# Performance work log

Hardware: AMD Instinct MI355X
Metric: run time of the kernel (lower is better)

The kernel has to match this reference:

```python
import jax, jax.numpy as jnp
import numpy as np

T, B, D, H = 4096, 4, 1024, 16


def setup_inputs() -> dict:
    key = jax.random.key(0)
    k0, k1, k2 = jax.random.split(key, 3)
    x = jax.random.normal(k0, (T, B, D), jnp.float32)
    Wqkv = jax.random.normal(k1, (3 * D, D), jnp.float32) * 0.02
    bqkv = jnp.zeros((3 * D,), jnp.float32)
    Wout = jax.random.normal(k2, (D, D), jnp.float32) * 0.02
    bout = jnp.zeros((D,), jnp.float32)
    return {"x": x, "Wqkv": Wqkv, "bqkv": bqkv, "Wout": Wout, "bout": bout, "nhead": H}


def reference(x, Wqkv, bqkv, Wout, bout, nhead):
    # x: (T, B, D) seq-first, query is key is value
    T_, B_, D_ = x.shape
    hd = D_ // nhead
    qkv = x @ Wqkv.T + bqkv                      # (T, B, 3D)
    q, k, v = jnp.split(qkv, 3, axis=-1)         # each (T, B, D)

    def heads(t):                                 # -> (B, H, T, hd)
        return t.reshape(T_, B_, nhead, hd).transpose(1, 2, 0, 3)

    q, k, v = heads(q), heads(k), heads(v)

    # Pearson correlation over the sequence axis: X, Y are (B, H, hd, T)
    X = jnp.swapaxes(q, -2, -1)
    Y = jnp.swapaxes(k, -2, -1)
    Xc = X - X.mean(-1, keepdims=True)
    Yc = Y - Y.mean(-1, keepdims=True)
    c = jnp.einsum('bhdt,bhet->bhde', Xc, Yc)    # (B, H, hd, hd)
    sx = (Xc ** 2).sum(-1)                       # (B, H, hd)
    sy = (Yc ** 2).sum(-1)                       # (B, H, hd)
    std = jnp.sqrt(sx[..., :, None] * sy[..., None, :])
    corr = jnp.clip(c / std, -1.0, 1.0)          # (B, H, hd, hd)

    attn = jnp.einsum('bhtd,bhde->bhte', v, corr)  # v @ corr: (B, H, T, hd)
    out = attn.transpose(2, 0, 1, 3).reshape(T_, B_, D_)  # (T, B, D)
    return out @ Wout.T + bout
```

## Files before the change

kernel.cpp:

```cpp
#include <hip/hip_runtime.h>
#include <hip/hip_bf16.h>

#define TDIM 4096
#define BDIM 4
#define DDIM 1024
#define HDIM 16
#define HD   64
#define MDIM (TDIM * BDIM)

typedef __attribute__((ext_vector_type(8))) short short8v;
typedef __attribute__((ext_vector_type(4))) float f32x4;

__device__ __forceinline__ ushort f2bfu(float f) {
  union { __hip_bfloat16 h; ushort u; } c;
  c.h = __float2bfloat16(f);
  return c.u;
}
__device__ __forceinline__ float bfu2f(ushort u) {
  union { ushort u; __hip_bfloat16 h; } c;
  c.u = u;
  return __bfloat162float(c.h);
}

#define GLOAD16(gp, lp) __builtin_amdgcn_global_load_lds( \
    (const __attribute__((address_space(1))) void*)(gp),  \
    (__attribute__((address_space(3))) void*)(lp), 16, 0, 0)

__global__ __launch_bounds__(256)
void split_f32(const float* __restrict__ in, ushort* __restrict__ hi,
               ushort* __restrict__ lo, int n4)
{
  int i = blockIdx.x * blockDim.x + threadIdx.x;
  const int stride = gridDim.x * blockDim.x;
  for (; i < n4; i += stride) {
    const float4 v = ((const float4*)in)[i];
    ushort4 h, l;
    h.x = f2bfu(v.x); l.x = f2bfu(v.x - bfu2f(h.x));
    h.y = f2bfu(v.y); l.y = f2bfu(v.y - bfu2f(h.y));
    h.z = f2bfu(v.z); l.z = f2bfu(v.z - bfu2f(h.z));
    h.w = f2bfu(v.w); l.w = f2bfu(v.w - bfu2f(h.w));
    ((ushort4*)hi)[i] = h;
    ((ushort4*)lo)[i] = l;
  }
}

__global__ __launch_bounds__(256, 2)
void gemm1_mfma(const float* __restrict__ X, const ushort* __restrict__ Wh,
                const ushort* __restrict__ Wl, const float* __restrict__ bias,
                float* __restrict__ QK, ushort* __restrict__ Vh,
                ushort* __restrict__ Vl)
{
  __shared__ ushort sAh[128][32], sAl[128][32], sBh[128][32], sBl[128][32];
  const int tid = threadIdx.x;
  const int lane = tid & 63, wid = tid >> 6;
  const int m0 = blockIdx.y * 128, n0 = blockIdx.x * 128;
  const int ar = tid >> 3, aq = tid & 7;
  const int wm = wid >> 1, wn = wid & 1;
  const int fr = lane & 15, kg = lane >> 4;

  f32x4 acc[4][4];
#pragma unroll
  for (int m = 0; m < 4; ++m)
#pragma unroll
    for (int n = 0; n < 4; ++n) acc[m][n] = (f32x4){0.f, 0.f, 0.f, 0.f};

  for (int k0 = 0; k0 < DDIM; k0 += 32) {
    float4 av[4];
#pragma unroll
    for (int i = 0; i < 4; ++i)
      av[i] = *(const float4*)&X[(size_t)(m0 + ar + i * 32) * DDIM + k0 + aq * 4];
#pragma unroll
    for (int j = 0; j < 4; ++j) {
      const int c = wid * 4 + j;
      const int r0 = (c & 7) * 16;
      const int row = r0 + (lane >> 2);
      const int s = lane & 3;
      const size_t goff = (size_t)(n0 + row) * DDIM + k0 + ((s ^ (row & 3)) << 3);
      if (c < 8) GLOAD16(Wh + goff, &sBh[r0][0]);
      else       GLOAD16(Wl + goff, &sBl[r0][0]);
    }
#pragma unroll
    for (int i = 0; i < 4; ++i) {
      const int row = ar + i * 32;
      const int sl = (((aq >> 1) ^ (row & 3)) << 3) + ((aq & 1) << 2);
      ushort4 hv, lv;
      hv.x = f2bfu(av[i].x); lv.x = f2bfu(av[i].x - bfu2f(hv.x));
      hv.y = f2bfu(av[i].y); lv.y = f2bfu(av[i].y - bfu2f(hv.y));
      hv.z = f2bfu(av[i].z); lv.z = f2bfu(av[i].z - bfu2f(hv.z));
      hv.w = f2bfu(av[i].w); lv.w = f2bfu(av[i].w - bfu2f(hv.w));
      *(ushort4*)&sAh[row][sl] = hv;
      *(ushort4*)&sAl[row][sl] = lv;
    }
    __syncthreads();

    short8v ah[4], al[4], bh[4], bl[4];
#pragma unroll
    for (int m = 0; m < 4; ++m) {
      const int row = wm * 64 + m * 16 + fr;
      const int so = (kg ^ (row & 3)) << 3;
      ah[m] = *(const short8v*)&sAh[row][so];
      al[m] = *(const short8v*)&sAl[row][so];
    }
#pragma unroll
    for (int n = 0; n < 4; ++n) {
      const int col = wn * 64 + n * 16 + fr;
      const int so = (kg ^ (col & 3)) << 3;
      bh[n] = *(const short8v*)&sBh[col][so];
      bl[n] = *(const short8v*)&sBl[col][so];
    }
#pragma unroll
    for (int m = 0; m < 4; ++m)
#pragma unroll
      for (int n = 0; n < 4; ++n) {
        acc[m][n] = __builtin_amdgcn_mfma_f32_16x16x32_bf16(ah[m], bh[n], acc[m][n], 0, 0, 0);
        acc[m][n] = __builtin_amdgcn_mfma_f32_16x16x32_bf16(ah[m], bl[n], acc[m][n], 0, 0, 0);
        acc[m][n] = __builtin_amdgcn_mfma_f32_16x16x32_bf16(al[m], bh[n], acc[m][n], 0, 0, 0);
      }
    __syncthreads();
  }

  const int isV = (n0 >= 2048);
#pragma unroll
  for (int m = 0; m < 4; ++m)
#pragma unroll
    for (int n = 0; n < 4; ++n) {
      const int col = n0 + wn * 64 + n * 16 + fr;
      const float bz = bias[col];
#pragma unroll
      for (int r = 0; r < 4; ++r) {
        const int row = m0 + wm * 64 + m * 16 + kg * 4 + r;
        const float v = acc[m][n][r] + bz;
        if (!isV) {
          QK[(size_t)row * 2048 + col] = v;
        } else {
          const size_t o = (size_t)row * 1024 + (col - 2048);
          const ushort h = f2bfu(v);
          Vh[o] = h;
          Vl[o] = f2bfu(v - bfu2f(h));
        }
      }
    }
}

__global__ __launch_bounds__(256, 2)
void gemm2_mfma(const ushort* __restrict__ Vh, const ushort* __restrict__ Vl,
                const ushort* __restrict__ Weh, const ushort* __restrict__ Wel,
                const float* __restrict__ bias, float* __restrict__ Out)
{
  __shared__ ushort sAh[128][32], sAl[128][32], sBh[128][32], sBl[128][32];
  const int tid = threadIdx.x;
  const int lane = tid & 63, wid = tid >> 6;
  const int m0 = blockIdx.y * 128, n0 = blockIdx.x * 128, bb = blockIdx.z;
  const int wm = wid >> 1, wn = wid & 1;
  const int fr = lane & 15, kg = lane >> 4;

  f32x4 acc[4][4];
#pragma unroll
  for (int m = 0; m < 4; ++m)
#pragma unroll
    for (int n = 0; n < 4; ++n) acc[m][n] = (f32x4){0.f, 0.f, 0.f, 0.f};

  const size_t wB = (size_t)bb * DDIM * DDIM;

  for (int k0 = 0; k0 < DDIM; k0 += 32) {
#pragma unroll
    for (int j = 0; j < 8; ++j) {
      const int r0 = j * 16;
      const int row = r0 + (lane >> 2);
      const int s = lane & 3;
      const int ks = k0 + ((s ^ (row & 3)) << 3);
      if (wid == 0)
        GLOAD16(Vh + (size_t)((m0 + row) * 4 + bb) * 1024 + ks, &sAh[r0][0]);
      else if (wid == 1)
        GLOAD16(Vl + (size_t)((m0 + row) * 4 + bb) * 1024 + ks, &sAl[r0][0]);
      else if (wid == 2)
        GLOAD16(Weh + wB + (size_t)(n0 + row) * 1024 + ks, &sBh[r0][0]);
      else
        GLOAD16(Wel + wB + (size_t)(n0 + row) * 1024 + ks, &sBl[r0][0]);
    }
    __syncthreads();

    short8v ah[4], al[4], bh[4], bl[4];
#pragma unroll
    for (int m = 0; m < 4; ++m) {
      const int row = wm * 64 + m * 16 + fr;
      const int so = (kg ^ (row & 3)) << 3;
      ah[m] = *(const short8v*)&sAh[row][so];
      al[m] = *(const short8v*)&sAl[row][so];
    }
#pragma unroll
    for (int n = 0; n < 4; ++n) {
      const int col = wn * 64 + n * 16 + fr;
      const int so = (kg ^ (col & 3)) << 3;
      bh[n] = *(const short8v*)&sBh[col][so];
      bl[n] = *(const short8v*)&sBl[col][so];
    }
#pragma unroll
    for (int m = 0; m < 4; ++m)
#pragma unroll
      for (int n = 0; n < 4; ++n) {
        acc[m][n] = __builtin_amdgcn_mfma_f32_16x16x32_bf16(ah[m], bh[n], acc[m][n], 0, 0, 0);
        acc[m][n] = __builtin_amdgcn_mfma_f32_16x16x32_bf16(ah[m], bl[n], acc[m][n], 0, 0, 0);
        acc[m][n] = __builtin_amdgcn_mfma_f32_16x16x32_bf16(al[m], bh[n], acc[m][n], 0, 0, 0);
      }
    __syncthreads();
  }

  float* Ob = Out + (size_t)bb * 1024;
#pragma unroll
  for (int m = 0; m < 4; ++m)
#pragma unroll
    for (int n = 0; n < 4; ++n) {
      const int col = n0 + wn * 64 + n * 16 + fr;
      const float bz = bias[col];
#pragma unroll
      for (int r = 0; r < 4; ++r) {
        const int row = m0 + wm * 64 + m * 16 + kg * 4 + r;
        Ob[(size_t)row * 4096 + col] = acc[m][n][r] + bz;
      }
    }
}

__global__ __launch_bounds__(64)
void corr_partial(const float* __restrict__ QK, float* __restrict__ P)
{
  __shared__ float qs[32][64];
  __shared__ float ks[32][64];
  const int bh  = blockIdx.x;
  const int seg = blockIdx.y;
  const int b = bh >> 4;
  const int h = bh & 15;
  const int lane = threadIdx.x;
  const float* qb = QK + (size_t)b * 2048 + h * HD;
  const float* kb = qb + 1024;
  const int ty = lane >> 3;
  const int tx = lane & 7;
  const int rr = lane >> 4;
  const int cq = lane & 15;

  float acc[8][8];
#pragma unroll
  for (int i = 0; i < 8; ++i)
#pragma unroll
    for (int j = 0; j < 8; ++j) acc[i][j] = 0.f;
  float sQ[4]  = {0,0,0,0}, sK[4]  = {0,0,0,0};
  float sQ2[4] = {0,0,0,0}, sK2[4] = {0,0,0,0};

  for (int c = 0; c < 8; ++c) {
    const int tbase = seg * 256 + c * 32;
    float4 qv[8], kv[8];
#pragma unroll
    for (int i = 0; i < 8; ++i) {
      const size_t g = (size_t)(tbase + rr + i*4) * 8192 + cq * 4;
      qv[i] = *(const float4*)&qb[g];
      kv[i] = *(const float4*)&kb[g];
    }
    __syncthreads();
#pragma unroll
    for (int i = 0; i < 8; ++i) {
      const int row = rr + i*4;
      *(float4*)&qs[row][cq*4] = qv[i];
      *(float4*)&ks[row][cq*4] = kv[i];
      sQ[0] += qv[i].x; sQ[1] += qv[i].y; sQ[2] += qv[i].z; sQ[3] += qv[i].w;
      sK[0] += kv[i].x; sK[1] += kv[i].y; sK[2] += kv[i].z; sK[3] += kv[i].w;
      sQ2[0] = fmaf(qv[i].x, qv[i].x, sQ2[0]); sQ2[1] = fmaf(qv[i].y, qv[i].y, sQ2[1]);
      sQ2[2] = fmaf(qv[i].z, qv[i].z, sQ2[2]); sQ2[3] = fmaf(qv[i].w, qv[i].w, sQ2[3]);
      sK2[0] = fmaf(kv[i].x, kv[i].x, sK2[0]); sK2[1] = fmaf(kv[i].y, kv[i].y, sK2[1]);
      sK2[2] = fmaf(kv[i].z, kv[i].z, sK2[2]); sK2[3] = fmaf(kv[i].w, kv[i].w, sK2[3]);
    }
    __syncthreads();
#pragma unroll 8
    for (int t = 0; t < 32; ++t) {
      const float4 qa  = *(const float4*)&qs[t][ty*8];
      const float4 qb4 = *(const float4*)&qs[t][ty*8+4];
      const float4 ka  = *(const float4*)&ks[t][tx*8];
      const float4 kb4 = *(const float4*)&ks[t][tx*8+4];
      const float av[8] = {qa.x, qa.y, qa.z, qa.w, qb4.x, qb4.y, qb4.z, qb4.w};
      const float bv[8] = {ka.x, ka.y, ka.z, ka.w, kb4.x, kb4.y, kb4.z, kb4.w};
#pragma unroll
      for (int i = 0; i < 8; ++i)
#pragma unroll
        for (int j = 0; j < 8; ++j)
          acc[i][j] = fmaf(av[i], bv[j], acc[i][j]);
    }
  }

#pragma unroll
  for (int j = 0; j < 4; ++j) {
    sQ[j]  += __shfl_xor(sQ[j], 16, 64);  sQ[j]  += __shfl_xor(sQ[j], 32, 64);
    sK[j]  += __shfl_xor(sK[j], 16, 64);  sK[j]  += __shfl_xor(sK[j], 32, 64);
    sQ2[j] += __shfl_xor(sQ2[j], 16, 64); sQ2[j] += __shfl_xor(sQ2[j], 32, 64);
    sK2[j] += __shfl_xor(sK2[j], 16, 64); sK2[j] += __shfl_xor(sK2[j], 32, 64);
  }

  float* Pb = P + (size_t)(bh * 16 + seg) * 4352;
#pragma unroll
  for (int i = 0; i < 8; ++i) {
    const int row = ty*8 + i;
    float4 o0, o1;
    o0.x = acc[i][0]; o0.y = acc[i][1]; o0.z = acc[i][2]; o0.w = acc[i][3];
    o1.x = acc[i][4]; o1.y = acc[i][5]; o1.z = acc[i][6]; o1.w = acc[i][7];
    *(float4*)&Pb[row*64 + tx*8]     = o0;
    *(float4*)&Pb[row*64 + tx*8 + 4] = o1;
  }
  if (lane < 16) {
    float4 q4; q4.x = sQ[0];  q4.y = sQ[1];  q4.z = sQ[2];  q4.w = sQ[3];
    float4 k4; k4.x = sK[0];  k4.y = sK[1];  k4.z = sK[2];  k4.w = sK[3];
    float4 q2; q2.x = sQ2[0]; q2.y = sQ2[1]; q2.z = sQ2[2]; q2.w = sQ2[3];
    float4 k2; k2.x = sK2[0]; k2.y = sK2[1]; k2.z = sK2[2]; k2.w = sK2[3];
    *(float4*)&Pb[4096 + lane*4] = q4;
    *(float4*)&Pb[4160 + lane*4] = k4;
    *(float4*)&Pb[4224 + lane*4] = q2;
    *(float4*)&Pb[4288 + lane*4] = k2;
  }
}

__global__ __launch_bounds__(256)
void corr_finalize(const float* __restrict__ P, float* __restrict__ corr)
{
  __shared__ float fin[4][64];
  const int bh = blockIdx.x;
  const int tid = threadIdx.x;
  const float* Pb = P + (size_t)bh * 16 * 4352;

  float s = 0.f;
  for (int seg = 0; seg < 16; ++seg) s += Pb[(size_t)seg*4352 + 4096 + tid];
  fin[tid >> 6][tid & 63] = s;

  float cacc[16];
#pragma unroll
  for (int i = 0; i < 16; ++i) cacc[i] = 0.f;
  for (int seg = 0; seg < 16; ++seg) {
#pragma unroll
    for (int i = 0; i < 16; ++i)
      cacc[i] += Pb[(size_t)seg*4352 + tid + i*256];
  }
  __syncthreads();

  const float invT = 1.0f / (float)TDIM;
#pragma unroll
  for (int i = 0; i < 16; ++i) {
    const int f = tid + i*256;
    const int d = f >> 6, e = f & 63;
    const float sq = fin[0][d], sk = fin[1][e];
    const float sq2 = fin[2][d], sk2 = fin[3][e];
    const float cc = cacc[i] - sq * sk * invT;
    const float sx = sq2 - sq * sq * invT;
    const float sy = sk2 - sk * sk * invT;
    float v = cc / sqrtf(sx * sy);
    v = fminf(1.f, fmaxf(-1.f, v));
    corr[(size_t)bh * 4096 + f] = v;
  }
}

__global__ __launch_bounds__(256)
void weff_kernel(const float* __restrict__ corr, const float* __restrict__ Wout,
                 float* __restrict__ Weff)
{
  __shared__ float cs[64][64];
  __shared__ float ws[128][64];
  const int bh = blockIdx.x;
  const int b = bh >> 4, h = bh & 15;
  const int n0 = blockIdx.y * 128;
  const int tid = threadIdx.x;

  const float* cb = corr + (size_t)bh * 4096;
  float4* csv = (float4*)&cs[0][0];
#pragma unroll
  for (int i = 0; i < 4; ++i)
    csv[tid + 256*i] = ((const float4*)cb)[tid + 256*i];

  const int wr = tid >> 1, wh = (tid & 1) * 32;
  const float* wrow = Wout + (size_t)(n0 + wr) * DDIM + h * HD + wh;
#pragma unroll
  for (int i = 0; i < 8; ++i)
    *(float4*)&ws[wr][wh + i*4] = *(const float4*)&wrow[i*4];
  __syncthreads();

  const int ni = (tid >> 3) * 4;
  const int di = (tid & 7) * 8;
  float acc[4][8];
#pragma unroll
  for (int i = 0; i < 4; ++i)
#pragma unroll
    for (int j = 0; j < 8; ++j) acc[i][j] = 0.f;

  for (int e = 0; e < 64; ++e) {
    float wv[4], cv[8];
#pragma unroll
    for (int i = 0; i < 4; ++i) wv[i] = ws[ni + i][e];
#pragma unroll
    for (int j = 0; j < 8; ++j) cv[j] = cs[di + j][e];
#pragma unroll
    for (int i = 0; i < 4; ++i)
#pragma unroll
      for (int j = 0; j < 8; ++j)
        acc[i][j] = fmaf(wv[i], cv[j], acc[i][j]);
  }

  float* Wb = Weff + (size_t)b * DDIM * DDIM + h * HD;
#pragma unroll
  for (int i = 0; i < 4; ++i) {
    float4 o0, o1;
    o0.x = acc[i][0]; o0.y = acc[i][1]; o0.z = acc[i][2]; o0.w = acc[i][3];
    o1.x = acc[i][4]; o1.y = acc[i][5]; o1.z = acc[i][6]; o1.w = acc[i][7];
    *(float4*)&Wb[(size_t)(n0 + ni + i) * DDIM + di]     = o0;
    *(float4*)&Wb[(size_t)(n0 + ni + i) * DDIM + di + 4] = o1;
  }
}

extern "C" void kernel_launch(void* const* d_in, const int* in_sizes, int n_in,
                              void* d_out, int out_size, void* d_ws, size_t ws_size,
                              hipStream_t stream)
{
  (void)in_sizes; (void)n_in; (void)out_size; (void)ws_size;
  const float* x    = (const float*)d_in[0];
  const float* Wqkv = (const float*)d_in[1];
  const float* bqkv = (const float*)d_in[2];
  const float* Wout = (const float*)d_in[3];
  const float* bout = (const float*)d_in[4];
  float* out = (float*)d_out;

  char* w = (char*)d_ws;
  float*  QK    = (float*)w;   w += (size_t)134217728;
  ushort* Vh    = (ushort*)w;  w += (size_t)33554432;
  ushort* Vl    = (ushort*)w;  w += (size_t)33554432;
  float*  corrB = (float*)w;   w += (size_t)1048576;
  char* R1 = w;                w += (size_t)17825792;
  char* R2 = w;
  ushort* Wqh   = (ushort*)R1;
  ushort* Wql   = Wqh + (size_t)3145728;
  float*  P     = (float*)R1;
  float*  WeffF = (float*)R1;
  ushort* Weh   = (ushort*)R2;
  ushort* Wel   = Weh + (size_t)4194304;

  split_f32<<<dim3(1024), 256, 0, stream>>>(Wqkv, Wqh, Wql, 786432);
  gemm1_mfma<<<dim3(24, 128), 256, 0, stream>>>(x, Wqh, Wql, bqkv, QK, Vh, Vl);
  corr_partial<<<dim3(64, 16), 64, 0, stream>>>(QK, P);
  corr_finalize<<<dim3(64), 256, 0, stream>>>(P, corrB);
  weff_kernel<<<dim3(64, 8), 256, 0, stream>>>(corrB, Wout, WeffF);
  split_f32<<<dim3(1024), 256, 0, stream>>>(WeffF, Weh, Wel, 1048576);
  gemm2_mfma<<<dim3(8, 32, 4), 256, 0, stream>>>(Vh, Vl, Weh, Wel, bout, out);
}
```

Baseline: 667.2 us.

## Split corr_partial across four waves and adjust LDS swizzle in GEMMs

corr_partial now runs 256 threads per block, with each wave handling its own quarter of the 256-row segment in private LDS tiles. The per-wave 64x64 partial products and sums are then reduced through shared memory before one coalesced write. The goal is to fill the GPU better, since the old kernel launched only 1024 single-wave blocks. Separately, the GEMM LDS XOR swizzle changes from row&3 to (row>>1)&3, to reduce bank conflicts on the 16-byte MFMA operand reads. The wave-serialized reduction adds syncs and LDS traffic.

```diff
diff --git a/kernel.cpp b/kernel.cpp
--- a/kernel.cpp
+++ b/kernel.cpp
@@ -25,6 +25,8 @@
 #define GLOAD16(gp, lp) __builtin_amdgcn_global_load_lds( \
     (const __attribute__((address_space(1))) void*)(gp),  \
     (__attribute__((address_space(3))) void*)(lp), 16, 0, 0)
+
+#define SWZ(row) (((row) >> 1) & 3)
 
 __global__ __launch_bounds__(256)
 void split_f32(const float* __restrict__ in, ushort* __restrict__ hi,
@@ -75,14 +77,14 @@
       const int r0 = (c & 7) * 16;
       const int row = r0 + (lane >> 2);
       const int s = lane & 3;
-      const size_t goff = (size_t)(n0 + row) * DDIM + k0 + ((s ^ (row & 3)) << 3);
+      const size_t goff = (size_t)(n0 + row) * DDIM + k0 + ((s ^ SWZ(row)) << 3);
       if (c < 8) GLOAD16(Wh + goff, &sBh[r0][0]);
       else       GLOAD16(Wl + goff, &sBl[r0][0]);
     }
 #pragma unroll
     for (int i = 0; i < 4; ++i) {
       const int row = ar + i * 32;
-      const int sl = (((aq >> 1) ^ (row & 3)) << 3) + ((aq & 1) << 2);
+      const int sl = (((aq >> 1) ^ SWZ(row)) << 3) + ((aq & 1) << 2);
       ushort4 hv, lv;
       hv.x = f2bfu(av[i].x); lv.x = f2bfu(av[i].x - bfu2f(hv.x));
       hv.y = f2bfu(av[i].y); lv.y = f2bfu(av[i].y - bfu2f(hv.y));
@@ -97,14 +99,14 @@
 #pragma unroll
     for (int m = 0; m < 4; ++m) {
       const int row = wm * 64 + m * 16 + fr;
-      const int so = (kg ^ (row & 3)) << 3;
+      const int so = (kg ^ SWZ(row)) << 3;
       ah[m] = *(const short8v*)&sAh[row][so];
       al[m] = *(const short8v*)&sAl[row][so];
     }
 #pragma unroll
     for (int n = 0; n < 4; ++n) {
       const int col = wn * 64 + n * 16 + fr;
-      const int so = (kg ^ (col & 3)) << 3;
+      const int so = (kg ^ SWZ(col)) << 3;
       bh[n] = *(const short8v*)&sBh[col][so];
       bl[n] = *(const short8v*)&sBl[col][so];
     }
@@ -168,7 +170,7 @@
       const int r0 = j * 16;
       const int row = r0 + (lane >> 2);
       const int s = lane & 3;
-      const int ks = k0 + ((s ^ (row & 3)) << 3);
+      const int ks = k0 + ((s ^ SWZ(row)) << 3);
       if (wid == 0)
         GLOAD16(Vh + (size_t)((m0 + row) * 4 + bb) * 1024 + ks, &sAh[r0][0]);
       else if (wid == 1)
@@ -184,14 +186,14 @@
 #pragma unroll
     for (int m = 0; m < 4; ++m) {
       const int row = wm * 64 + m * 16 + fr;
-      const int so = (kg ^ (row & 3)) << 3;
+      const int so = (kg ^ SWZ(row)) << 3;
       ah[m] = *(const short8v*)&sAh[row][so];
       al[m] = *(const short8v*)&sAl[row][so];
     }
 #pragma unroll
     for (int n = 0; n < 4; ++n) {
       const int col = wn * 64 + n * 16 + fr;
-      const int so = (kg ^ (col & 3)) << 3;
+      const int so = (kg ^ SWZ(col)) << 3;
       bh[n] = *(const short8v*)&sBh[col][so];
       bl[n] = *(const short8v*)&sBl[col][so];
     }
@@ -221,16 +223,18 @@
     }
 }
 
-__global__ __launch_bounds__(64)
+__global__ __launch_bounds__(256)
 void corr_partial(const float* __restrict__ QK, float* __restrict__ P)
 {
-  __shared__ float qs[32][64];
-  __shared__ float ks[32][64];
+  __shared__ float qs[4][16][64];
+  __shared__ float ks[4][16][64];
+  __shared__ float ssum[4][4][64];
   const int bh  = blockIdx.x;
   const int seg = blockIdx.y;
   const int b = bh >> 4;
   const int h = bh & 15;
-  const int lane = threadIdx.x;
+  const int tid = threadIdx.x;
+  const int wid = tid >> 6, lane = tid & 63;
   const float* qb = QK + (size_t)b * 2048 + h * HD;
   const float* kb = qb + 1024;
   const int ty = lane >> 3;
@@ -246,21 +250,20 @@
   float sQ[4]  = {0,0,0,0}, sK[4]  = {0,0,0,0};
   float sQ2[4] = {0,0,0,0}, sK2[4] = {0,0,0,0};
 
-  for (int c = 0; c < 8; ++c) {
-    const int tbase = seg * 256 + c * 32;
-    float4 qv[8], kv[8];
-#pragma unroll
-    for (int i = 0; i < 8; ++i) {
+  for (int c = 0; c < 4; ++c) {
+    const int tbase = seg * 256 + wid * 64 + c * 16;
+    float4 qv[4], kv[4];
+#pragma unroll
+    for (int i = 0; i < 4; ++i) {
       const size_t g = (size_t)(tbase + rr + i*4) * 8192 + cq * 4;
       qv[i] = *(const float4*)&qb[g];
       kv[i] = *(const float4*)&kb[g];
     }
-    __syncthreads();
-#pragma unroll
-    for (int i = 0; i < 8; ++i) {
+#pragma unroll
+    for (int i = 0; i < 4; ++i) {
       const int row = rr + i*4;
-      *(float4*)&qs[row][cq*4] = qv[i];
-      *(float4*)&ks[row][cq*4] = kv[i];
+      *(float4*)&qs[wid][row][cq*4] = qv[i];
+      *(float4*)&ks[wid][row][cq*4] = kv[i];
       sQ[0] += qv[i].x; sQ[1] += qv[i].y; sQ[2] += qv[i].z; sQ[3] += qv[i].w;
       sK[0] += kv[i].x; sK[1] += kv[i].y; sK[2] += kv[i].z; sK[3] += kv[i].w;
       sQ2[0] = fmaf(qv[i].x, qv[i].x, sQ2[0]); sQ2[1] = fmaf(qv[i].y, qv[i].y, sQ2[1]);
@@ -268,13 +271,12 @@
       sK2[0] = fmaf(kv[i].x, kv[i].x, sK2[0]); sK2[1] = fmaf(kv[i].y, kv[i].y, sK2[1]);
       sK2[2] = fmaf(kv[i].z, kv[i].z, sK2[2]); sK2[3] = fmaf(kv[i].w, kv[i].w, sK2[3]);
     }
-    __syncthreads();
 #pragma unroll 8
-    for (int t = 0; t < 32; ++t) {
-      const float4 qa  = *(const float4*)&qs[t][ty*8];
-      const float4 qb4 = *(const float4*)&qs[t][ty*8+4];
-      const float4 ka  = *(const float4*)&ks[t][tx*8];
-      const float4 kb4 = *(const float4*)&ks[t][tx*8+4];
+    for (int t = 0; t < 16; ++t) {
+      const float4 qa  = *(const float4*)&qs[wid][t][ty*8];
+      const float4 qb4 = *(const float4*)&qs[wid][t][ty*8+4];
+      const float4 ka  = *(const float4*)&ks[wid][t][tx*8];
+      const float4 kb4 = *(const float4*)&ks[wid][t][tx*8+4];
       const float av[8] = {qa.x, qa.y, qa.z, qa.w, qb4.x, qb4.y, qb4.z, qb4.w};
       const float bv[8] = {ka.x, ka.y, ka.z, ka.w, kb4.x, kb4.y, kb4.z, kb4.w};
 #pragma unroll
@@ -292,26 +294,49 @@
     sQ2[j] += __shfl_xor(sQ2[j], 16, 64); sQ2[j] += __shfl_xor(sQ2[j], 32, 64);
     sK2[j] += __shfl_xor(sK2[j], 16, 64); sK2[j] += __shfl_xor(sK2[j], 32, 64);
   }
-
-  float* Pb = P + (size_t)(bh * 16 + seg) * 4352;
-#pragma unroll
-  for (int i = 0; i < 8; ++i) {
-    const int row = ty*8 + i;
-    float4 o0, o1;
-    o0.x = acc[i][0]; o0.y = acc[i][1]; o0.z = acc[i][2]; o0.w = acc[i][3];
-    o1.x = acc[i][4]; o1.y = acc[i][5]; o1.z = acc[i][6]; o1.w = acc[i][7];
-    *(float4*)&Pb[row*64 + tx*8]     = o0;
-    *(float4*)&Pb[row*64 + tx*8 + 4] = o1;
-  }
   if (lane < 16) {
     float4 q4; q4.x = sQ[0];  q4.y = sQ[1];  q4.z = sQ[2];  q4.w = sQ[3];
     float4 k4; k4.x = sK[0];  k4.y = sK[1];  k4.z = sK[2];  k4.w = sK[3];
     float4 q2; q2.x = sQ2[0]; q2.y = sQ2[1]; q2.z = sQ2[2]; q2.w = sQ2[3];
     float4 k2; k2.x = sK2[0]; k2.y = sK2[1]; k2.z = sK2[2]; k2.w = sK2[3];
-    *(float4*)&Pb[4096 + lane*4] = q4;
-    *(float4*)&Pb[4160 + lane*4] = k4;
-    *(float4*)&Pb[4224 + lane*4] = q2;
-    *(float4*)&Pb[4288 + lane*4] = k2;
+    *(float4*)&ssum[wid][0][lane*4] = q4;
+    *(float4*)&ssum[wid][1][lane*4] = k4;
+    *(float4*)&ssum[wid][2][lane*4] = q2;
+    *(float4*)&ssum[wid][3][lane*4] = k2;
+  }
+
+  float* cbuf = &qs[0][0][0];
+  __syncthreads();
+#pragma unroll
+  for (int w = 0; w < 4; ++w) {
+    if (wid == w) {
+#pragma unroll
+      for (int i = 0; i < 8; ++i) {
+        float* p0 = &cbuf[(ty*8 + i) * 64 + tx*8];
+        if (w == 0) {
+          float4 o0, o1;
+          o0.x = acc[i][0]; o0.y = acc[i][1]; o0.z = acc[i][2]; o0.w = acc[i][3];
+          o1.x = acc[i][4]; o1.y = acc[i][5]; o1.z = acc[i][6]; o1.w = acc[i][7];
+          *(float4*)p0 = o0; *(float4*)(p0 + 4) = o1;
+        } else {
+          float4 o0 = *(const float4*)p0, o1 = *(const float4*)(p0 + 4);
+          o0.x += acc[i][0]; o0.y += acc[i][1]; o0.z += acc[i][2]; o0.w += acc[i][3];
+          o1.x += acc[i][4]; o1.y += acc[i][5]; o1.z += acc[i][6]; o1.w += acc[i][7];
+          *(float4*)p0 = o0; *(float4*)(p0 + 4) = o1;
+        }
+      }
+    }
+    __syncthreads();
+  }
+
+  float* Pb = P + (size_t)(bh * 16 + seg) * 4352;
+#pragma unroll
+  for (int i = 0; i < 4; ++i)
+    ((float4*)Pb)[tid + 256*i] = ((const float4*)cbuf)[tid + 256*i];
+  {
+    const int comp = tid >> 6, d = tid & 63;
+    Pb[4096 + tid] = ssum[0][comp][d] + ssum[1][comp][d] +
+                     ssum[2][comp][d] + ssum[3][comp][d];
   }
 }
 
@@ -437,7 +462,7 @@
 
   split_f32<<<dim3(1024), 256, 0, stream>>>(Wqkv, Wqh, Wql, 786432);
   gemm1_mfma<<<dim3(24, 128), 256, 0, stream>>>(x, Wqh, Wql, bqkv, QK, Vh, Vl);
-  corr_partial<<<dim3(64, 16), 64, 0, stream>>>(QK, P);
+  corr_partial<<<dim3(64, 16), 256, 0, stream>>>(QK, P);
   corr_finalize<<<dim3(64), 256, 0, stream>>>(P, corrB);
   weff_kernel<<<dim3(64, 8), 256, 0, stream>>>(corrB, Wout, WeffF);
   split_f32<<<dim3(1024), 256, 0, stream>>>(WeffF, Weh, Wel, 1048576);
```

Result: no change. 659.2 us (-1.2%).
